# Kernel optimization log

Measured on AMD Instinct MI355X. Metric: run time of the kernel, lower is better.

Reference implementation:

```python
import jax, jax.numpy as jnp
import numpy as np

B, P, Q, D = 16, 4096, 1024, 256


def setup_inputs() -> dict:
    key = jax.random.key(0)
    k1, k2, k3, k4 = jax.random.split(key, 4)
    return {
        "passage_encodes": jax.random.normal(k1, (B, P, D), dtype=jnp.float32),
        "question_encodes": jax.random.normal(k2, (B, Q, D), dtype=jnp.float32),
        "w_attn": jax.random.normal(k3, (2 * D, 1), dtype=jnp.float32) * (1.0 / np.sqrt(2 * D)),
        "b_attn": jnp.zeros((1,), dtype=jnp.float32),
        "w_out": jax.random.normal(k4, (2 * D, 256), dtype=jnp.float32) * (1.0 / np.sqrt(2 * D)),
        "b_out": jnp.zeros((256,), dtype=jnp.float32),
    }


def reference(passage_encodes, question_encodes, w_attn, b_attn, w_out, b_out):
    # similarity matrix [B, P, Q]
    sim = jnp.einsum('bpd,bqd->bpq', passage_encodes, question_encodes)
    # context-to-question attention
    c2q = jax.nn.softmax(sim, axis=-1)                       # [B, P, Q]
    ctx2q = jnp.einsum('bpq,bqd->bpd', c2q, question_encodes)  # [B, P, D]
    # question-to-context attention (softmax over row-max)
    q2c = jax.nn.softmax(jnp.max(sim, axis=-1), axis=-1)     # [B, P]
    q2c_vec = jnp.einsum('bp,bpd->bd', q2c, passage_encodes)  # [B, D]
    tp = jnp.tanh(passage_encodes)
    concat = jnp.concatenate([
        tp * jnp.tanh(ctx2q),
        tp * jnp.tanh(q2c_vec)[:, None, :],  # broadcast instead of repeat
    ], axis=-1)                                              # [B, P, 2D]
    # attention reducer: linear -> softmax over sequence -> weighted sum
    w = jax.nn.softmax(jnp.einsum('bpc,co->bp', concat, w_attn) + b_attn[0], axis=1)
    reduced = jnp.einsum('bp,bpc->bc', w, concat)            # [B, 2D]
    return reduced @ w_out + b_out                            # [B, output_dim]
```

## Files before the change

kernel.cpp:

```cpp
#include <hip/hip_runtime.h>
#include <cmath>

#define BB 16
#define PP 4096
#define QQ 1024
#define DD 256

typedef __attribute__((ext_vector_type(8))) short short8;
typedef __attribute__((ext_vector_type(4))) float floatx4;
typedef __attribute__((ext_vector_type(4))) _Float16 half4;

static __device__ inline ushort bf16_rne(float x) {
  unsigned u = __float_as_uint(x);
  unsigned r = (u + 0x7fffu + ((u >> 16) & 1u)) >> 16;
  return (ushort)r;
}
static __device__ inline float bf16f(ushort h) { return __uint_as_float(((unsigned)h) << 16); }

static __device__ inline float ftanh(float x) {
  float e = __expf(2.0f * x);
  return 1.0f - 2.0f * __builtin_amdgcn_rcpf(e + 1.0f);
}

static __device__ inline void gl16(const void* g, void* l) {
  __builtin_amdgcn_global_load_lds(
      (const __attribute__((address_space(1))) unsigned int*)g,
      (__attribute__((address_space(3))) unsigned int*)l, 16, 0, 0);
}

__global__ __launch_bounds__(256) void kQprep(
    const float* __restrict__ ques, ushort* __restrict__ qb)
{
  const int b = blockIdx.y, qt = blockIdx.x;
  __shared__ float tile[32][260];
  const int tid = threadIdx.x;
  const float* src = ques + ((size_t)b * QQ + qt * 32) * DD;
  for (int i = tid; i < 32 * 64; i += 256) {
    int r = i >> 6, c = (i & 63) << 2;
    *(float4*)&tile[r][c] = *(const float4*)(src + r * DD + c);
  }
  __syncthreads();
  ushort* blob = qb + (size_t)(b * 32 + qt) * 24576;
  {
    int r = tid >> 3;
    int j0 = (tid & 7) * 4;
#pragma unroll
    for (int jj = 0; jj < 4; ++jj) {
      int j = j0 + jj;
      ushort h8[8], l8[8];
#pragma unroll
      for (int e = 0; e < 8; ++e) {
        float x = tile[r][j * 8 + e];
        ushort h = bf16_rne(x);
        h8[e] = h; l8[e] = bf16_rne(x - bf16f(h));
      }
      int g = r * 32 + (j ^ (r & 7));
      *(uint4*)&blob[(size_t)g * 8] = *(uint4*)h8;
      *(uint4*)&blob[8192 + (size_t)g * 8] = *(uint4*)l8;
    }
  }
  {
    int d = tid;
    int s = (d >> 1) & 3;
    ushort h32[32];
#pragma unroll
    for (int r = 0; r < 32; ++r) h32[r] = bf16_rne(tile[r][d]);
#pragma unroll
    for (int k = 0; k < 4; ++k)
      *(uint4*)&blob[16384 + (size_t)d * 32 + (k ^ s) * 8] = *(uint4*)&h32[k * 8];
  }
}

__global__ __launch_bounds__(512, 1) void kA(
    const float* __restrict__ pass, const ushort* __restrict__ qb,
    const float* __restrict__ w_attn,
    _Float16* __restrict__ first_h, _Float16* __restrict__ tp_h,
    float* __restrict__ rowmax, float* __restrict__ logit1)
{
  __shared__ alignas(16) char sm[147456];

  const int b    = blockIdx.y;
  const int p0   = blockIdx.x * 128;
  const int tid  = threadIdx.x;
  const int w    = tid >> 6;
  const int lane = tid & 63;
  const int l15  = lane & 15;
  const int quad = lane >> 4;
  const int swz  = l15 & 7;

  short8 bhi[8], blo[8];
  {
    const float* prow = pass + (((size_t)b * PP + p0 + w * 16 + l15) * DD);
#pragma unroll
    for (int c = 0; c < 8; ++c) {
      const float* p8 = prow + c * 32 + quad * 8;
      float4 x0 = *(const float4*)p8;
      float4 x1 = *(const float4*)(p8 + 4);
      float xs[8] = {x0.x, x0.y, x0.z, x0.w, x1.x, x1.y, x1.z, x1.w};
#pragma unroll
      for (int j = 0; j < 8; ++j) {
        ushort h = bf16_rne(xs[j]);
        ushort lo = bf16_rne(xs[j] - bf16f(h));
        bhi[c][j] = (short)h;
        blo[c][j] = (short)lo;
      }
    }
  }

  int goff[8];
#pragma unroll
  for (int c = 0; c < 8; ++c) goff[c] = (l15 * 32 + ((4 * c + quad) ^ swz)) * 8;
  const int vtoff = l15 * 32 + ((quad ^ ((l15 >> 1) & 3)) * 8);

  const ushort* tb = qb + (size_t)b * 32 * 24576;
  const int dma_l = w * 3072 + lane * 8;
  const int dma_s = w * 6144 + lane * 16;

  floatx4 accO[16];
#pragma unroll
  for (int i = 0; i < 16; ++i) accO[i] = (floatx4){0.f, 0.f, 0.f, 0.f};
  float mx = -INFINITY, ps = 0.f;
  short8 phi = {0, 0, 0, 0, 0, 0, 0, 0}, plo = {0, 0, 0, 0, 0, 0, 0, 0};

  {
    const ushort* gs = tb + dma_l;
    char* ld = sm + dma_s;
#pragma unroll
    for (int i = 0; i < 6; ++i) gl16(gs + i * 512, ld + i * 1024);
  }
  __syncthreads();

  for (int t = 0; t < 32; ++t) {
    const int ic = t % 3, ip = (t + 2) % 3, inx = (t + 1) % 3;
    char* cur = sm + ic * 49152;
    char* prv = sm + ip * 49152;
    if (t < 31) {
      const ushort* gs = tb + (size_t)(t + 1) * 24576 + dma_l;
      char* ld = sm + inx * 49152 + dma_s;
#pragma unroll
      for (int i = 0; i < 6; ++i) gl16(gs + i * 512, ld + i * 1024);
    }

    const ushort* Qhi = (const ushort*)cur;
    const ushort* Qlo = (const ushort*)(cur + 16384);
    floatx4 s0 = (floatx4){0.f, 0.f, 0.f, 0.f};
    floatx4 s1 = (floatx4){0.f, 0.f, 0.f, 0.f};
#pragma unroll
    for (int c = 0; c < 8; ++c) {
      short8 a0h = *(const short8*)&Qhi[goff[c]];
      short8 a0l = *(const short8*)&Qlo[goff[c]];
      short8 a1h = *(const short8*)&Qhi[goff[c] + 4096];
      short8 a1l = *(const short8*)&Qlo[goff[c] + 4096];
      s0 = __builtin_amdgcn_mfma_f32_16x16x32_bf16(a0h, bhi[c], s0, 0, 0, 0);
      s0 = __builtin_amdgcn_mfma_f32_16x16x32_bf16(a0h, blo[c], s0, 0, 0, 0);
      s0 = __builtin_amdgcn_mfma_f32_16x16x32_bf16(a0l, bhi[c], s0, 0, 0, 0);
      s1 = __builtin_amdgcn_mfma_f32_16x16x32_bf16(a1h, bhi[c], s1, 0, 0, 0);
      s1 = __builtin_amdgcn_mfma_f32_16x16x32_bf16(a1h, blo[c], s1, 0, 0, 0);
      s1 = __builtin_amdgcn_mfma_f32_16x16x32_bf16(a1l, bhi[c], s1, 0, 0, 0);
    }

    if (t > 0) {
      const ushort* TQ = (const ushort*)(prv + 32768);
#pragma unroll
      for (int nt = 0; nt < 16; ++nt) {
        short8 vhi = *(const short8*)&TQ[nt * 512 + vtoff];
        accO[nt] = __builtin_amdgcn_mfma_f32_16x16x32_bf16(phi, vhi, accO[nt], 0, 0, 0);
        accO[nt] = __builtin_amdgcn_mfma_f32_16x16x32_bf16(plo, vhi, accO[nt], 0, 0, 0);
      }
    }

    float pv[8];
#pragma unroll
    for (int r = 0; r < 4; ++r) {
      float s = s0[r];
      mx = fmaxf(mx, s);
      pv[r] = __expf(s - 60.f);
      ps += pv[r];
    }
#pragma unroll
    for (int r = 0; r < 4; ++r) {
      float s = s1[r];
      mx = fmaxf(mx, s);
      pv[4 + r] = __expf(s - 60.f);
      ps += pv[4 + r];
    }

    unsigned* pwv = (unsigned*)prv + w * 512;
#pragma unroll
    for (int mt = 0; mt < 2; ++mt) {
      unsigned pk[4];
#pragma unroll
      for (int r = 0; r < 4; ++r) {
        float x = pv[mt * 4 + r];
        ushort h = bf16_rne(x);
        ushort lo = bf16_rne(x - bf16f(h));
        pk[r] = (unsigned)h | ((unsigned)lo << 16);
      }
      int g = l15 * 8 + ((mt * 4 + quad) ^ swz);
      *(uint4*)&pwv[g * 4] = *(uint4*)pk;
    }
    uint4 u0 = *(const uint4*)&pwv[(l15 * 8 + ((2 * quad) ^ swz)) * 4];
    uint4 u1 = *(const uint4*)&pwv[(l15 * 8 + ((2 * quad + 1) ^ swz)) * 4];
    unsigned ua[8] = {u0.x, u0.y, u0.z, u0.w, u1.x, u1.y, u1.z, u1.w};
#pragma unroll
    for (int j = 0; j < 8; ++j) {
      phi[j] = (short)(ua[j] & 0xffffu);
      plo[j] = (short)(ua[j] >> 16);
    }
    __syncthreads();
  }

  {
    const ushort* TQ = (const ushort*)(sm + 49152 + 32768);
#pragma unroll
    for (int nt = 0; nt < 16; ++nt) {
      short8 vhi = *(const short8*)&TQ[nt * 512 + vtoff];
      accO[nt] = __builtin_amdgcn_mfma_f32_16x16x32_bf16(phi, vhi, accO[nt], 0, 0, 0);
      accO[nt] = __builtin_amdgcn_mfma_f32_16x16x32_bf16(plo, vhi, accO[nt], 0, 0, 0);
    }
  }

  ps += __shfl_xor(ps, 16);
  ps += __shfl_xor(ps, 32);
  mx = fmaxf(mx, __shfl_xor(mx, 16));
  mx = fmaxf(mx, __shfl_xor(mx, 32));

  __syncthreads();
  float* Of = (float*)(sm + w * 16640);
#pragma unroll
  for (int nt = 0; nt < 16; ++nt)
#pragma unroll
    for (int r = 0; r < 4; ++r)
      Of[(quad * 4 + r) * 260 + nt * 16 + l15] = accO[nt][r];
  const float4 w1 = *(const float4*)(w_attn + lane * 4);
  const size_t rowoff = (size_t)b * PP + p0 + w * 16;
#pragma unroll
  for (int j = 0; j < 16; ++j) {
    float4 o = *(const float4*)&Of[j * 260 + lane * 4];
    float linv = 1.f / __shfl(ps, j);
    float4 pv4 = *(const float4*)(pass + (rowoff + j) * DD + lane * 4);
    float tpx = ftanh(pv4.x), tpy = ftanh(pv4.y), tpz = ftanh(pv4.z), tpw = ftanh(pv4.w);
    float4 f;
    f.x = tpx * ftanh(o.x * linv);
    f.y = tpy * ftanh(o.y * linv);
    f.z = tpz * ftanh(o.z * linv);
    f.w = tpw * ftanh(o.w * linv);
    half4 fh = {(_Float16)f.x, (_Float16)f.y, (_Float16)f.z, (_Float16)f.w};
    half4 th = {(_Float16)tpx, (_Float16)tpy, (_Float16)tpz, (_Float16)tpw};
    *(half4*)(first_h + (rowoff + j) * DD + lane * 4) = fh;
    *(half4*)(tp_h + (rowoff + j) * DD + lane * 4) = th;
    float part = f.x * w1.x + f.y * w1.y + f.z * w1.z + f.w * w1.w;
    part += __shfl_xor(part, 1);  part += __shfl_xor(part, 2);
    part += __shfl_xor(part, 4);  part += __shfl_xor(part, 8);
    part += __shfl_xor(part, 16); part += __shfl_xor(part, 32);
    if (lane == 0) logit1[rowoff + j] = part;
  }
  if (lane < 16) rowmax[rowoff + lane] = mx;
}

__global__ __launch_bounds__(256) void kB2(
    const float* __restrict__ pass, const float* __restrict__ rowmax,
    float* __restrict__ numpart, float* __restrict__ denpart)
{
  const int b = blockIdx.y, chunk = blockIdx.x;
  const int tid = threadIdx.x, r = tid >> 6, ln = tid & 63;
  __shared__ float sacc[4][64][4];
  __shared__ float sden[4][64];
  const float* rm = rowmax + (size_t)b * PP + chunk * 128;
  const float* pb = pass + ((size_t)b * PP + chunk * 128) * DD;
  float4 acc = make_float4(0.f, 0.f, 0.f, 0.f);
  float den = 0.f;
  for (int p = r; p < 128; p += 4) {
    float wgt = __expf(rm[p] - 60.f);
    float4 v = *(const float4*)(pb + (size_t)p * DD + ln * 4);
    acc.x += wgt * v.x; acc.y += wgt * v.y;
    acc.z += wgt * v.z; acc.w += wgt * v.w;
    den += wgt;
  }
  *(float4*)&sacc[r][ln][0] = acc;
  sden[r][ln] = den;
  __syncthreads();
  if (r == 0) {
    float4 s;
    s.x = sacc[0][ln][0] + sacc[1][ln][0] + sacc[2][ln][0] + sacc[3][ln][0];
    s.y = sacc[0][ln][1] + sacc[1][ln][1] + sacc[2][ln][1] + sacc[3][ln][1];
    s.z = sacc[0][ln][2] + sacc[1][ln][2] + sacc[2][ln][2] + sacc[3][ln][2];
    s.w = sacc[0][ln][3] + sacc[1][ln][3] + sacc[2][ln][3] + sacc[3][ln][3];
    *(float4*)(numpart + (size_t)(chunk * 16 + b) * DD + ln * 4) = s;
    if (ln == 0)
      denpart[chunk * 16 + b] = sden[0][0] + sden[1][0] + sden[2][0] + sden[3][0];
  }
}

__global__ void kB3(const float* __restrict__ numpart, const float* __restrict__ denpart,
                    const float* __restrict__ w_attn,
                    float* __restrict__ tq, float* __restrict__ w2tq)
{
  const int b = blockIdx.x, d = threadIdx.x;
  float den = 0.f, num = 0.f;
#pragma unroll
  for (int c = 0; c < 32; ++c) {
    den += denpart[c * 16 + b];
    num += numpart[(size_t)(c * 16 + b) * DD + d];
  }
  float t = ftanh(num / den);
  tq[b * DD + d] = t;
  w2tq[b * DD + d] = w_attn[DD + d] * t;
}

__global__ __launch_bounds__(256) void kC(
    const _Float16* __restrict__ tp_h, const float* __restrict__ logit1,
    const float* __restrict__ w2tq, float* __restrict__ el)
{
  const int b = blockIdx.y, chunk = blockIdx.x;
  const int wave = threadIdx.x >> 6, lane = threadIdx.x & 63;
  const float4 wv = *(const float4*)(w2tq + b * DD + (lane << 2));
  const int pbase = chunk * 128 + wave * 32;
  for (int j = 0; j < 32; ++j) {
    int p = pbase + j;
    half4 tv = *(const half4*)(tp_h + ((size_t)b * PP + p) * DD + (lane << 2));
    float part = (float)tv.x * wv.x + (float)tv.y * wv.y +
                 (float)tv.z * wv.z + (float)tv.w * wv.w;
    part += __shfl_xor(part, 1);  part += __shfl_xor(part, 2);
    part += __shfl_xor(part, 4);  part += __shfl_xor(part, 8);
    part += __shfl_xor(part, 16); part += __shfl_xor(part, 32);
    if (lane == 0)
      el[(size_t)b * PP + p] = __expf(logit1[(size_t)b * PP + p] + part);
  }
}

__global__ __launch_bounds__(256) void kE(
    const _Float16* __restrict__ tp_h, const _Float16* __restrict__ first_h,
    const float* __restrict__ el,
    float* __restrict__ r1part, float* __restrict__ r2part, float* __restrict__ den2part)
{
  const int b = blockIdx.y, chunk = blockIdx.x;
  const int tid = threadIdx.x, r = tid >> 6, ln = tid & 63;
  __shared__ float s1[4][64][4];
  __shared__ float s2[4][64][4];
  __shared__ float sd[4][64];
  const float* ev = el + (size_t)b * PP + chunk * 128;
  const size_t base = ((size_t)b * PP + chunk * 128) * DD;
  float a1[4] = {0.f, 0.f, 0.f, 0.f}, a2[4] = {0.f, 0.f, 0.f, 0.f};
  float den = 0.f;
  for (int p = r; p < 128; p += 4) {
    float wgt = ev[p];
    half4 f = *(const half4*)(first_h + base + (size_t)p * DD + ln * 4);
    half4 t = *(const half4*)(tp_h + base + (size_t)p * DD + ln * 4);
    a1[0] += wgt * (float)f.x; a1[1] += wgt * (float)f.y;
    a1[2] += wgt * (float)f.z; a1[3] += wgt * (float)f.w;
    a2[0] += wgt * (float)t.x; a2[1] += wgt * (float)t.y;
    a2[2] += wgt * (float)t.z; a2[3] += wgt * (float)t.w;
    den += wgt;
  }
  *(float4*)&s1[r][ln][0] = *(float4*)a1;
  *(float4*)&s2[r][ln][0] = *(float4*)a2;
  sd[r][ln] = den;
  __syncthreads();
  if (r == 0) {
    float o1[4], o2[4];
#pragma unroll
    for (int i = 0; i < 4; ++i) {
      o1[i] = s1[0][ln][i] + s1[1][ln][i] + s1[2][ln][i] + s1[3][ln][i];
      o2[i] = s2[0][ln][i] + s2[1][ln][i] + s2[2][ln][i] + s2[3][ln][i];
    }
    *(float4*)(r1part + (size_t)(chunk * 16 + b) * DD + ln * 4) = *(float4*)o1;
    *(float4*)(r2part + (size_t)(chunk * 16 + b) * DD + ln * 4) = *(float4*)o2;
    if (ln == 0)
      den2part[chunk * 16 + b] = sd[0][0] + sd[1][0] + sd[2][0] + sd[3][0];
  }
}

__global__ __launch_bounds__(256) void kF(
    const float* __restrict__ r1part, const float* __restrict__ r2part,
    const float* __restrict__ den2part, const float* __restrict__ tq,
    const float* __restrict__ w_out, const float* __restrict__ b_out,
    float* __restrict__ out)
{
  const int b = blockIdx.x, o = threadIdx.x;
  __shared__ float R1[256], R2[256];
  float den = 0.f, red1 = 0.f, red2 = 0.f;
#pragma unroll
  for (int c = 0; c < 32; ++c) {
    den += den2part[c * 16 + b];
    red1 += r1part[(size_t)(c * 16 + b) * DD + o];
    red2 += r2part[(size_t)(c * 16 + b) * DD + o];
  }
  float inv = 1.f / den;
  R1[o] = red1 * inv;
  R2[o] = red2 * inv * tq[b * DD + o];
  __syncthreads();
  float acc = b_out[o];
  for (int k = 0; k < DD; ++k)
    acc += R1[k] * w_out[k * 256 + o];
  for (int k = 0; k < DD; ++k)
    acc += R2[k] * w_out[(DD + k) * 256 + o];
  out[b * 256 + o] = acc;
}

extern "C" void kernel_launch(void* const* d_in, const int* in_sizes, int n_in,
                              void* d_out, int out_size, void* d_ws, size_t ws_size,
                              hipStream_t stream) {
  const float* pass   = (const float*)d_in[0];
  const float* ques   = (const float*)d_in[1];
  const float* w_attn = (const float*)d_in[2];
  const float* w_out  = (const float*)d_in[4];
  const float* b_out  = (const float*)d_in[5];
  float* out = (float*)d_out;

  float* ws       = (float*)d_ws;
  float* rowmax   = ws;
  float* logit1   = rowmax   + (size_t)BB * PP;
  float* el       = logit1   + (size_t)BB * PP;
  float* numpart  = el       + (size_t)BB * PP;
  float* denpart  = numpart  + (size_t)32 * BB * DD;
  float* r1part   = denpart  + 32 * BB;
  float* r2part   = r1part   + (size_t)32 * BB * DD;
  float* den2part = r2part   + (size_t)32 * BB * DD;
  float* tq       = den2part + 32 * BB;
  float* w2tq     = tq       + BB * DD;
  ushort* qbb     = (ushort*)(w2tq + BB * DD);
  _Float16* first_h = (_Float16*)(qbb + (size_t)BB * 32 * 24576);
  _Float16* tp_h    = first_h + (size_t)BB * PP * DD;

  kQprep<<<dim3(QQ / 32, BB), 256, 0, stream>>>(ques, qbb);
  kA    <<<dim3(PP / 128, BB), 512, 0, stream>>>(pass, qbb, w_attn,
                                                 first_h, tp_h, rowmax, logit1);
  kB2   <<<dim3(32, BB), 256, 0, stream>>>(pass, rowmax, numpart, denpart);
  kB3   <<<BB, 256, 0, stream>>>(numpart, denpart, w_attn, tq, w2tq);
  kC    <<<dim3(32, BB), 256, 0, stream>>>(tp_h, logit1, w2tq, el);
  kE    <<<dim3(32, BB), 256, 0, stream>>>(tp_h, first_h, el, r1part, r2part, den2part);
  kF    <<<BB, 256, 0, stream>>>(r1part, r2part, den2part, tq, w_out, b_out, out);
}
```

Measured before the change: 352.4 us.

## Fuse q2c reduction into kA, merge kC into kE, load V from global

The q2c weighted sum over passage rows (formerly kB2) now runs in kA's epilogue using the row max held in registers, so the rowmax buffer and a second pass over the passage are gone. kC's logit computation is folded into kE, which now reads tp_h once with half8 loads. The value (transposed Q) tile is no longer staged through LDS. It is loaded straight from global into registers one iteration ahead, which cuts the LDS DMA per tile and frees LDS for the P exchange. Launch bounds now request 2 blocks per SM, though the 144KB static LDS likely still limits kA to one block.

```diff
diff --git a/kernel.cpp b/kernel.cpp
--- a/kernel.cpp
+++ b/kernel.cpp
@@ -9,6 +9,7 @@
 typedef __attribute__((ext_vector_type(8))) short short8;
 typedef __attribute__((ext_vector_type(4))) float floatx4;
 typedef __attribute__((ext_vector_type(4))) _Float16 half4;
+typedef __attribute__((ext_vector_type(8))) _Float16 half8;
 
 static __device__ inline ushort bf16_rne(float x) {
   unsigned u = __float_as_uint(x);
@@ -61,21 +62,21 @@
   }
   {
     int d = tid;
-    int s = (d >> 1) & 3;
     ushort h32[32];
 #pragma unroll
     for (int r = 0; r < 32; ++r) h32[r] = bf16_rne(tile[r][d]);
 #pragma unroll
     for (int k = 0; k < 4; ++k)
-      *(uint4*)&blob[16384 + (size_t)d * 32 + (k ^ s) * 8] = *(uint4*)&h32[k * 8];
-  }
-}
-
-__global__ __launch_bounds__(512, 1) void kA(
+      *(uint4*)&blob[16384 + (size_t)d * 32 + k * 8] = *(uint4*)&h32[k * 8];
+  }
+}
+
+__global__ __launch_bounds__(512, 2) void kA(
     const float* __restrict__ pass, const ushort* __restrict__ qb,
     const float* __restrict__ w_attn,
     _Float16* __restrict__ first_h, _Float16* __restrict__ tp_h,
-    float* __restrict__ rowmax, float* __restrict__ logit1)
+    float* __restrict__ logit1,
+    float* __restrict__ numpart, float* __restrict__ denpart)
 {
   __shared__ alignas(16) char sm[147456];
 
@@ -110,23 +111,24 @@
   int goff[8];
 #pragma unroll
   for (int c = 0; c < 8; ++c) goff[c] = (l15 * 32 + ((4 * c + quad) ^ swz)) * 8;
-  const int vtoff = l15 * 32 + ((quad ^ ((l15 >> 1) & 3)) * 8);
 
   const ushort* tb = qb + (size_t)b * 32 * 24576;
-  const int dma_l = w * 3072 + lane * 8;
-  const int dma_s = w * 6144 + lane * 16;
+  const int dma_g = (w >> 2) * 8192 + (w & 3) * 2048 + lane * 8;
+  const int dma_s = (w >> 2) * 16384 + (w & 3) * 4096 + lane * 16;
+  const ushort* vbase = tb + 16384 + l15 * 32 + quad * 8;
 
   floatx4 accO[16];
 #pragma unroll
   for (int i = 0; i < 16; ++i) accO[i] = (floatx4){0.f, 0.f, 0.f, 0.f};
   float mx = -INFINITY, ps = 0.f;
   short8 phi = {0, 0, 0, 0, 0, 0, 0, 0}, plo = {0, 0, 0, 0, 0, 0, 0, 0};
+  short8 vreg[16];
 
   {
-    const ushort* gs = tb + dma_l;
+    const ushort* gs = tb + dma_g;
     char* ld = sm + dma_s;
 #pragma unroll
-    for (int i = 0; i < 6; ++i) gl16(gs + i * 512, ld + i * 1024);
+    for (int i = 0; i < 4; ++i) gl16(gs + i * 512, ld + i * 1024);
   }
   __syncthreads();
 
@@ -135,10 +137,18 @@
     char* cur = sm + ic * 49152;
     char* prv = sm + ip * 49152;
     if (t < 31) {
-      const ushort* gs = tb + (size_t)(t + 1) * 24576 + dma_l;
+      const ushort* gs = tb + (size_t)(t + 1) * 24576 + dma_g;
       char* ld = sm + inx * 49152 + dma_s;
 #pragma unroll
-      for (int i = 0; i < 6; ++i) gl16(gs + i * 512, ld + i * 1024);
+      for (int i = 0; i < 4; ++i) gl16(gs + i * 512, ld + i * 1024);
+    }
+
+    if (t > 0) {
+#pragma unroll
+      for (int nt = 0; nt < 16; ++nt) {
+        accO[nt] = __builtin_amdgcn_mfma_f32_16x16x32_bf16(phi, vreg[nt], accO[nt], 0, 0, 0);
+        accO[nt] = __builtin_amdgcn_mfma_f32_16x16x32_bf16(plo, vreg[nt], accO[nt], 0, 0, 0);
+      }
     }
 
     const ushort* Qhi = (const ushort*)cur;
@@ -159,14 +169,10 @@
       s1 = __builtin_amdgcn_mfma_f32_16x16x32_bf16(a1l, bhi[c], s1, 0, 0, 0);
     }
 
-    if (t > 0) {
-      const ushort* TQ = (const ushort*)(prv + 32768);
-#pragma unroll
-      for (int nt = 0; nt < 16; ++nt) {
-        short8 vhi = *(const short8*)&TQ[nt * 512 + vtoff];
-        accO[nt] = __builtin_amdgcn_mfma_f32_16x16x32_bf16(phi, vhi, accO[nt], 0, 0, 0);
-        accO[nt] = __builtin_amdgcn_mfma_f32_16x16x32_bf16(plo, vhi, accO[nt], 0, 0, 0);
-      }
+    {
+      const ushort* vt = vbase + (size_t)t * 24576;
+#pragma unroll
+      for (int nt = 0; nt < 16; ++nt) vreg[nt] = *(const short8*)(vt + nt * 512);
     }
 
     float pv[8];
@@ -185,7 +191,7 @@
       ps += pv[4 + r];
     }
 
-    unsigned* pwv = (unsigned*)prv + w * 512;
+    unsigned* pwv = (unsigned*)(prv + 32768) + w * 512;
 #pragma unroll
     for (int mt = 0; mt < 2; ++mt) {
       unsigned pk[4];
@@ -210,14 +216,10 @@
     __syncthreads();
   }
 
-  {
-    const ushort* TQ = (const ushort*)(sm + 49152 + 32768);
-#pragma unroll
-    for (int nt = 0; nt < 16; ++nt) {
-      short8 vhi = *(const short8*)&TQ[nt * 512 + vtoff];
-      accO[nt] = __builtin_amdgcn_mfma_f32_16x16x32_bf16(phi, vhi, accO[nt], 0, 0, 0);
-      accO[nt] = __builtin_amdgcn_mfma_f32_16x16x32_bf16(plo, vhi, accO[nt], 0, 0, 0);
-    }
+#pragma unroll
+  for (int nt = 0; nt < 16; ++nt) {
+    accO[nt] = __builtin_amdgcn_mfma_f32_16x16x32_bf16(phi, vreg[nt], accO[nt], 0, 0, 0);
+    accO[nt] = __builtin_amdgcn_mfma_f32_16x16x32_bf16(plo, vreg[nt], accO[nt], 0, 0, 0);
   }
 
   ps += __shfl_xor(ps, 16);
@@ -234,11 +236,17 @@
       Of[(quad * 4 + r) * 260 + nt * 16 + l15] = accO[nt][r];
   const float4 w1 = *(const float4*)(w_attn + lane * 4);
   const size_t rowoff = (size_t)b * PP + p0 + w * 16;
+  float aq[4] = {0.f, 0.f, 0.f, 0.f};
+  float dq = 0.f;
 #pragma unroll
   for (int j = 0; j < 16; ++j) {
     float4 o = *(const float4*)&Of[j * 260 + lane * 4];
     float linv = 1.f / __shfl(ps, j);
     float4 pv4 = *(const float4*)(pass + (rowoff + j) * DD + lane * 4);
+    float wq = __expf(__shfl(mx, j) - 60.f);
+    aq[0] += wq * pv4.x; aq[1] += wq * pv4.y;
+    aq[2] += wq * pv4.z; aq[3] += wq * pv4.w;
+    dq += wq;
     float tpx = ftanh(pv4.x), tpy = ftanh(pv4.y), tpz = ftanh(pv4.z), tpw = ftanh(pv4.w);
     float4 f;
     f.x = tpx * ftanh(o.x * linv);
@@ -255,40 +263,22 @@
     part += __shfl_xor(part, 16); part += __shfl_xor(part, 32);
     if (lane == 0) logit1[rowoff + j] = part;
   }
-  if (lane < 16) rowmax[rowoff + lane] = mx;
-}
-
-__global__ __launch_bounds__(256) void kB2(
-    const float* __restrict__ pass, const float* __restrict__ rowmax,
-    float* __restrict__ numpart, float* __restrict__ denpart)
-{
-  const int b = blockIdx.y, chunk = blockIdx.x;
-  const int tid = threadIdx.x, r = tid >> 6, ln = tid & 63;
-  __shared__ float sacc[4][64][4];
-  __shared__ float sden[4][64];
-  const float* rm = rowmax + (size_t)b * PP + chunk * 128;
-  const float* pb = pass + ((size_t)b * PP + chunk * 128) * DD;
-  float4 acc = make_float4(0.f, 0.f, 0.f, 0.f);
-  float den = 0.f;
-  for (int p = r; p < 128; p += 4) {
-    float wgt = __expf(rm[p] - 60.f);
-    float4 v = *(const float4*)(pb + (size_t)p * DD + ln * 4);
-    acc.x += wgt * v.x; acc.y += wgt * v.y;
-    acc.z += wgt * v.z; acc.w += wgt * v.w;
-    den += wgt;
-  }
-  *(float4*)&sacc[r][ln][0] = acc;
-  sden[r][ln] = den;
-  __syncthreads();
-  if (r == 0) {
-    float4 s;
-    s.x = sacc[0][ln][0] + sacc[1][ln][0] + sacc[2][ln][0] + sacc[3][ln][0];
-    s.y = sacc[0][ln][1] + sacc[1][ln][1] + sacc[2][ln][1] + sacc[3][ln][1];
-    s.z = sacc[0][ln][2] + sacc[1][ln][2] + sacc[2][ln][2] + sacc[3][ln][2];
-    s.w = sacc[0][ln][3] + sacc[1][ln][3] + sacc[2][ln][3] + sacc[3][ln][3];
-    *(float4*)(numpart + (size_t)(chunk * 16 + b) * DD + ln * 4) = s;
-    if (ln == 0)
-      denpart[chunk * 16 + b] = sden[0][0] + sden[1][0] + sden[2][0] + sden[3][0];
+  float* QP = (float*)(sm + 133120);
+  float* QD = (float*)(sm + 141312);
+  *(float4*)&QP[w * 256 + lane * 4] = make_float4(aq[0], aq[1], aq[2], aq[3]);
+  if (lane == 0) QD[w] = dq;
+  __syncthreads();
+  if (tid < 256) {
+    float s = 0.f;
+#pragma unroll
+    for (int j = 0; j < 8; ++j) s += QP[j * 256 + tid];
+    numpart[(size_t)(blockIdx.x * 16 + b) * DD + tid] = s;
+  }
+  if (tid == 0) {
+    float s = 0.f;
+#pragma unroll
+    for (int j = 0; j < 8; ++j) s += QD[j];
+    denpart[blockIdx.x * 16 + b] = s;
   }
 }
 
@@ -308,66 +298,59 @@
   w2tq[b * DD + d] = w_attn[DD + d] * t;
 }
 
-__global__ __launch_bounds__(256) void kC(
-    const _Float16* __restrict__ tp_h, const float* __restrict__ logit1,
-    const float* __restrict__ w2tq, float* __restrict__ el)
-{
-  const int b = blockIdx.y, chunk = blockIdx.x;
-  const int wave = threadIdx.x >> 6, lane = threadIdx.x & 63;
-  const float4 wv = *(const float4*)(w2tq + b * DD + (lane << 2));
-  const int pbase = chunk * 128 + wave * 32;
-  for (int j = 0; j < 32; ++j) {
-    int p = pbase + j;
-    half4 tv = *(const half4*)(tp_h + ((size_t)b * PP + p) * DD + (lane << 2));
-    float part = (float)tv.x * wv.x + (float)tv.y * wv.y +
-                 (float)tv.z * wv.z + (float)tv.w * wv.w;
-    part += __shfl_xor(part, 1);  part += __shfl_xor(part, 2);
-    part += __shfl_xor(part, 4);  part += __shfl_xor(part, 8);
-    part += __shfl_xor(part, 16); part += __shfl_xor(part, 32);
-    if (lane == 0)
-      el[(size_t)b * PP + p] = __expf(logit1[(size_t)b * PP + p] + part);
-  }
-}
-
 __global__ __launch_bounds__(256) void kE(
     const _Float16* __restrict__ tp_h, const _Float16* __restrict__ first_h,
-    const float* __restrict__ el,
+    const float* __restrict__ logit1, const float* __restrict__ w2tq,
     float* __restrict__ r1part, float* __restrict__ r2part, float* __restrict__ den2part)
 {
   const int b = blockIdx.y, chunk = blockIdx.x;
-  const int tid = threadIdx.x, r = tid >> 6, ln = tid & 63;
-  __shared__ float s1[4][64][4];
-  __shared__ float s2[4][64][4];
-  __shared__ float sd[4][64];
-  const float* ev = el + (size_t)b * PP + chunk * 128;
-  const size_t base = ((size_t)b * PP + chunk * 128) * DD;
-  float a1[4] = {0.f, 0.f, 0.f, 0.f}, a2[4] = {0.f, 0.f, 0.f, 0.f};
+  const int tid = threadIdx.x;
+  const int j = tid >> 5;
+  const int ln = tid & 31;
+  __shared__ float s1[8][256];
+  __shared__ float s2[8][256];
+  __shared__ float sd[8];
+  float w2[8];
+  *(float4*)&w2[0] = *(const float4*)(w2tq + b * DD + ln * 8);
+  *(float4*)&w2[4] = *(const float4*)(w2tq + b * DD + ln * 8 + 4);
+  float a1[8] = {0.f, 0.f, 0.f, 0.f, 0.f, 0.f, 0.f, 0.f};
+  float a2[8] = {0.f, 0.f, 0.f, 0.f, 0.f, 0.f, 0.f, 0.f};
   float den = 0.f;
-  for (int p = r; p < 128; p += 4) {
-    float wgt = ev[p];
-    half4 f = *(const half4*)(first_h + base + (size_t)p * DD + ln * 4);
-    half4 t = *(const half4*)(tp_h + base + (size_t)p * DD + ln * 4);
-    a1[0] += wgt * (float)f.x; a1[1] += wgt * (float)f.y;
-    a1[2] += wgt * (float)f.z; a1[3] += wgt * (float)f.w;
-    a2[0] += wgt * (float)t.x; a2[1] += wgt * (float)t.y;
-    a2[2] += wgt * (float)t.z; a2[3] += wgt * (float)t.w;
-    den += wgt;
-  }
-  *(float4*)&s1[r][ln][0] = *(float4*)a1;
-  *(float4*)&s2[r][ln][0] = *(float4*)a2;
-  sd[r][ln] = den;
-  __syncthreads();
-  if (r == 0) {
-    float o1[4], o2[4];
-#pragma unroll
-    for (int i = 0; i < 4; ++i) {
-      o1[i] = s1[0][ln][i] + s1[1][ln][i] + s1[2][ln][i] + s1[3][ln][i];
-      o2[i] = s2[0][ln][i] + s2[1][ln][i] + s2[2][ln][i] + s2[3][ln][i];
-    }
-    *(float4*)(r1part + (size_t)(chunk * 16 + b) * DD + ln * 4) = *(float4*)o1;
-    *(float4*)(r2part + (size_t)(chunk * 16 + b) * DD + ln * 4) = *(float4*)o2;
-    if (ln == 0)
-      den2part[chunk * 16 + b] = sd[0][0] + sd[1][0] + sd[2][0] + sd[3][0];
+  const size_t rowbase = (size_t)b * PP + chunk * 128;
+  for (int p = j; p < 128; p += 8) {
+    size_t gp = rowbase + p;
+    half8 t8 = *(const half8*)(tp_h + gp * DD + ln * 8);
+    float part = 0.f;
+#pragma unroll
+    for (int k = 0; k < 8; ++k) part += (float)t8[k] * w2[k];
+    part += __shfl_xor(part, 1); part += __shfl_xor(part, 2);
+    part += __shfl_xor(part, 4); part += __shfl_xor(part, 8);
+    part += __shfl_xor(part, 16);
+    float el = __expf(logit1[gp] + part);
+    half8 f8 = *(const half8*)(first_h + gp * DD + ln * 8);
+#pragma unroll
+    for (int k = 0; k < 8; ++k) {
+      a1[k] += el * (float)f8[k];
+      a2[k] += el * (float)t8[k];
+    }
+    den += el;
+  }
+  *(float4*)&s1[j][ln * 8]     = *(float4*)&a1[0];
+  *(float4*)&s1[j][ln * 8 + 4] = *(float4*)&a1[4];
+  *(float4*)&s2[j][ln * 8]     = *(float4*)&a2[0];
+  *(float4*)&s2[j][ln * 8 + 4] = *(float4*)&a2[4];
+  if (ln == 0) sd[j] = den;
+  __syncthreads();
+  float t1 = 0.f, t2 = 0.f;
+#pragma unroll
+  for (int q = 0; q < 8; ++q) { t1 += s1[q][tid]; t2 += s2[q][tid]; }
+  r1part[(size_t)(chunk * 16 + b) * DD + tid] = t1;
+  r2part[(size_t)(chunk * 16 + b) * DD + tid] = t2;
+  if (tid == 0) {
+    float s = 0.f;
+#pragma unroll
+    for (int q = 0; q < 8; ++q) s += sd[q];
+    den2part[chunk * 16 + b] = s;
   }
 }
 
@@ -409,10 +392,8 @@
   float* out = (float*)d_out;
 
   float* ws       = (float*)d_ws;
-  float* rowmax   = ws;
-  float* logit1   = rowmax   + (size_t)BB * PP;
-  float* el       = logit1   + (size_t)BB * PP;
-  float* numpart  = el       + (size_t)BB * PP;
+  float* logit1   = ws;
+  float* numpart  = logit1   + (size_t)BB * PP;
   float* denpart  = numpart  + (size_t)32 * BB * DD;
   float* r1part   = denpart  + 32 * BB;
   float* r2part   = r1part   + (size_t)32 * BB * DD;
@@ -424,11 +405,10 @@
   _Float16* tp_h    = first_h + (size_t)BB * PP * DD;
 
   kQprep<<<dim3(QQ / 32, BB), 256, 0, stream>>>(ques, qbb);
-  kA    <<<dim3(PP / 128, BB), 512, 0, stream>>>(pass, qbb, w_attn,
-                                                 first_h, tp_h, rowmax, logit1);
-  kB2   <<<dim3(32, BB), 256, 0, stream>>>(pass, rowmax, numpart, denpart);
+  kA    <<<dim3(PP / 128, BB), 512, 0, stream>>>(pass, qbb, w_attn, first_h, tp_h,
+                                                 logit1, numpart, denpart);
   kB3   <<<BB, 256, 0, stream>>>(numpart, denpart, w_attn, tq, w2tq);
-  kC    <<<dim3(32, BB), 256, 0, stream>>>(tp_h, logit1, w2tq, el);
-  kE    <<<dim3(32, BB), 256, 0, stream>>>(tp_h, first_h, el, r1part, r2part, den2part);
+  kE    <<<dim3(32, BB), 256, 0, stream>>>(tp_h, first_h, logit1, w2tq,
+                                           r1part, r2part, den2part);
   kF    <<<BB, 256, 0, stream>>>(r1part, r2part, den2part, tq, w_out, b_out, out);
 }
```

Measured after the change: 388.4 us. 1.1x slower.
